# Optimization experiments

Measured on AMD Instinct MI355X. Metric: run time of the kernel, lower is better.

The kernel has to match this reference:

```python
import jax, jax.numpy as jnp
import numpy as np

IN_FEATURES = 1024
N_CLASSES = 50257
CUTOFFS = [2000, 10000]      # head covers [0,2000); clusters [2000,10000), [10000,50257)
DIV_VALUE = 4.0
IGNORE_INDEX = -1
N_ROWS = 4096
HEAD_SIZE = CUTOFFS[0] + len(CUTOFFS)  # 2002 (head classes + one slot per tail cluster)
HSZ = [int(IN_FEATURES // (DIV_VALUE ** (i + 1))) for i in range(len(CUTOFFS))]  # [256, 64]
BOUNDS = CUTOFFS + [N_CLASSES]


def setup_inputs() -> dict:
    key = jax.random.key(0)
    ks = jax.random.split(key, 8)
    x = jax.random.normal(ks[0], (N_ROWS, IN_FEATURES), dtype=jnp.float32)
    target = jax.random.randint(ks[1], (N_ROWS,), 0, N_CLASSES, dtype=jnp.int64)
    drop = jax.random.uniform(ks[2], (N_ROWS,)) < 0.1
    target = jnp.where(drop, IGNORE_INDEX, target)
    s = 1.0 / np.sqrt(IN_FEATURES)
    head_w = jax.random.normal(ks[3], (HEAD_SIZE, IN_FEATURES), dtype=jnp.float32) * s
    proj0 = jax.random.normal(ks[4], (HSZ[0], IN_FEATURES), dtype=jnp.float32) * s
    out0 = jax.random.normal(ks[5], (BOUNDS[1] - BOUNDS[0], HSZ[0]), dtype=jnp.float32) * (1.0 / np.sqrt(HSZ[0]))
    proj1 = jax.random.normal(ks[6], (HSZ[1], IN_FEATURES), dtype=jnp.float32) * s
    out1 = jax.random.normal(ks[7], (BOUNDS[2] - BOUNDS[1], HSZ[1]), dtype=jnp.float32) * (1.0 / np.sqrt(HSZ[1]))
    return {"x": x, "target": target, "head_w": head_w,
            "proj0": proj0, "out0": out0, "proj1": proj1, "out1": out1}


def reference(x, target, head_w, proj0, out0, proj1, out1):
    # head: [N, cutoff0 + n_clusters] logits, shared log-softmax
    head_lp = jax.nn.log_softmax(jnp.einsum('nd,hd->nh', x, head_w), axis=-1)
    rows = jnp.arange(x.shape[0])
    valid = target != IGNORE_INDEX
    t = jnp.where(valid, target, 0)

    # head-band targets: log prob directly from head
    t_head = jnp.clip(t, 0, CUTOFFS[0] - 1)
    logp = head_lp[rows, t_head]

    # tail clusters: head cluster-slot logprob + within-cluster logprob
    tails = [(proj0, out0), (proj1, out1)]
    for i, (proj, out) in enumerate(tails):
        low, high = BOUNDS[i], BOUNDS[i + 1]
        # [N, hsz] @ [hsz, osz] -> [N, osz] cluster logits
        cl_lp = jax.nn.log_softmax(
            jnp.einsum('nh,oh->no', jnp.einsum('nd,hd->nh', x, proj), out), axis=-1)
        rel = jnp.clip(t - low, 0, high - low - 1)
        cand = head_lp[:, CUTOFFS[0] + i] + cl_lp[rows, rel]
        logp = jnp.where((t >= low) & (t < high), cand, logp)

    # ignore-index filter + mean == masked mean over valid rows
    vf = valid.astype(logp.dtype)
    loss = -(logp * vf).sum() / vf.sum()
    return loss
```

## Files before the change

### kernel.cpp

```cpp
#include <hip/hip_runtime.h>
#include <hip/hip_bf16.h>

typedef __attribute__((ext_vector_type(8))) short bf16x8;
typedef __attribute__((ext_vector_type(4))) float f32x4;
typedef unsigned short u16;

constexpr int NR      = 4096;
constexpr int INF     = 1024;
constexpr int HEAD_N  = 2002;
constexpr int HEAD_NP = 2048;
constexpr int C0_LO   = 2000, C0_HI = 10000;
constexpr int C0_N    = 8000;
constexpr int C1_N    = 40257;
constexpr int C1_NP   = 40320;
constexpr int K0      = 256;
constexpr int K1      = 64;
constexpr int PCAT    = 320;
constexpr int PCAT_P  = 384;
constexpr int WCAT_R  = HEAD_NP + PCAT_P;
constexpr int IGNORE  = -1;
constexpr float LOG2E = 1.4426950408889634f;
constexpr float LN2   = 0.6931471805599453f;

constexpr int S0      = 50;
constexpr int TPS0    = 5;
constexpr int S1      = 64;
constexpr int TPS1    = 5;
constexpr int NHP     = 32;
constexpr int HEADB   = 512;
constexpr int C1SLOTS = 768;
constexpr int C0SLOTS = 256;
constexpr int MEGA_GRID = HEADB + C1SLOTS + C0SLOTS;

static __device__ __forceinline__ u16 f32_to_bf16(float f) {
    unsigned int u = __float_as_uint(f);
    return (u16)((u + 0x7FFFu + ((u >> 16) & 1u)) >> 16);
}
static __device__ __forceinline__ float bf2f(u16 v) {
    unsigned int u = ((unsigned int)v) << 16;
    return __uint_as_float(u);
}

static __device__ __forceinline__ float fast_exp2(float x) {
#if __has_builtin(__builtin_amdgcn_exp2f)
    return __builtin_amdgcn_exp2f(x);
#else
    return __expf(x * LN2);
#endif
}

static __device__ __forceinline__ void gload_lds16(const u16* g, u16* l) {
    __builtin_amdgcn_global_load_lds(
        (const __attribute__((address_space(1))) unsigned int*)g,
        (__attribute__((address_space(3))) unsigned int*)l, 16, 0, 0);
}

struct CvtSegs { const float* s[6]; u16* d[6]; int n8[6]; float sc[6]; };

__global__ void cvt_compact(CvtSegs segs, const int* __restrict__ tgt,
                            int* __restrict__ c0list, int* __restrict__ c1list,
                            int* __restrict__ crow, int* __restrict__ cnts) {
    if (blockIdx.x == 0) {
        __shared__ int b0s, b1s;
        const int tid = threadIdx.x;
        const int lane = tid & 63;
        if (tid == 0) { b0s = 0; b1s = 0; }
        __syncthreads();
        for (int it = 0; it < NR / 256; ++it) {
            const int r = it * 256 + tid;
            const int t = tgt[r];
            const bool in0 = (t >= C0_LO) && (t < C0_HI);
            const bool in1 = (t >= C0_HI);
            unsigned long long m0 = __ballot(in0);
            unsigned long long m1 = __ballot(in1);
            int base0 = 0, base1 = 0;
            if (lane == 0) {
                base0 = atomicAdd(&b0s, (int)__popcll(m0));
                base1 = atomicAdd(&b1s, (int)__popcll(m1));
            }
            base0 = __shfl(base0, 0, 64);
            base1 = __shfl(base1, 0, 64);
            const unsigned long long lt = (1ULL << lane) - 1ULL;
            if (in0) { int s = base0 + (int)__popcll(m0 & lt); c0list[s] = r; crow[r] = s; }
            else if (in1) { int s = base1 + (int)__popcll(m1 & lt); c1list[s] = r; crow[r] = s; }
            else crow[r] = 0;
        }
        __syncthreads();
        const int c0 = b0s, c1 = b1s;
        const int p0 = (c0 + 127) & ~127;
        const int p1 = (c1 + 255) & ~255;
        if (threadIdx.x == 0) { cnts[0] = c0; cnts[1] = c1; cnts[2] = p0; cnts[3] = p1; }
        for (int i = c0 + (int)threadIdx.x; i < p0; i += 256) c0list[i] = 0;
        for (int i = c1 + (int)threadIdx.x; i < p1; i += 256) c1list[i] = 0;
    }

    const int stride = gridDim.x * blockDim.x;
    const int gid = blockIdx.x * blockDim.x + threadIdx.x;
#pragma unroll
    for (int seg = 0; seg < 6; ++seg) {
        const float4* sp = (const float4*)segs.s[seg];
        bf16x8* dp = (bf16x8*)segs.d[seg];
        const int n8 = segs.n8[seg];
        const float sc = segs.sc[seg];
        for (int i = gid; i < n8; i += stride) {
            float4 a = sp[2 * i], b = sp[2 * i + 1];
            bf16x8 o;
            o[0] = (short)f32_to_bf16(a.x * sc); o[1] = (short)f32_to_bf16(a.y * sc);
            o[2] = (short)f32_to_bf16(a.z * sc); o[3] = (short)f32_to_bf16(a.w * sc);
            o[4] = (short)f32_to_bf16(b.x * sc); o[5] = (short)f32_to_bf16(b.y * sc);
            o[6] = (short)f32_to_bf16(b.z * sc); o[7] = (short)f32_to_bf16(b.w * sc);
            dp[i] = o;
        }
    }
}

__launch_bounds__(256, 2)
__global__ void proj_tile(const u16* __restrict__ A, const u16* __restrict__ B,
                          u16* __restrict__ HB)
{
    constexpr int K = INF;
    __shared__ u16 ldsA[128 * 64];
    __shared__ u16 ldsB[128 * 64];
    const int tid = threadIdx.x, wid = tid >> 6, lane = tid & 63;
    const int wr = wid >> 1, wc = wid & 1;
    const int row0 = blockIdx.x * 128, col0 = blockIdx.y * 128;

    f32x4 acc[4][4];
#pragma unroll
    for (int m = 0; m < 4; ++m)
#pragma unroll
        for (int n = 0; n < 4; ++n) acc[m][n] = (f32x4){0.f, 0.f, 0.f, 0.f};

    const int srow = lane >> 3;
    const int ssw  = (lane & 7) ^ srow;

    for (int ks = 0; ks < K / 64; ++ks) {
        const int k0 = ks * 64;
#pragma unroll
        for (int q = 0; q < 4; ++q) {
            const int c = q * 4 + wid, row = c * 8 + srow;
            gload_lds16(A + (size_t)(row0 + row) * K + k0 + ssw * 8, ldsA + c * 512);
        }
#pragma unroll
        for (int q = 0; q < 4; ++q) {
            const int c = q * 4 + wid, row = c * 8 + srow;
            gload_lds16(B + (size_t)(col0 + row) * K + k0 + ssw * 8, ldsB + c * 512);
        }
        __syncthreads();
        const bf16x8* A8 = (const bf16x8*)ldsA;
        const bf16x8* B8 = (const bf16x8*)ldsB;
        bf16x8 af[4][2], bfr[4][2];
#pragma unroll
        for (int m = 0; m < 4; ++m) {
            const int ar = wr * 64 + m * 16 + (lane & 15);
#pragma unroll
            for (int ks2 = 0; ks2 < 2; ++ks2)
                af[m][ks2] = A8[ar * 8 + ((ks2 * 4 + (lane >> 4)) ^ (ar & 7))];
        }
#pragma unroll
        for (int n = 0; n < 4; ++n) {
            const int br = wc * 64 + n * 16 + (lane & 15);
#pragma unroll
            for (int ks2 = 0; ks2 < 2; ++ks2)
                bfr[n][ks2] = B8[br * 8 + ((ks2 * 4 + (lane >> 4)) ^ (br & 7))];
        }
#pragma unroll
        for (int ks2 = 0; ks2 < 2; ++ks2)
#pragma unroll
            for (int m = 0; m < 4; ++m)
#pragma unroll
                for (int n = 0; n < 4; ++n)
                    acc[m][n] = __builtin_amdgcn_mfma_f32_16x16x32_bf16(
                        af[m][ks2], bfr[n][ks2], acc[m][n], 0, 0, 0);
        __syncthreads();
    }
#pragma unroll
    for (int m = 0; m < 4; ++m)
#pragma unroll
        for (int n = 0; n < 4; ++n) {
            const int col = col0 + wc * 64 + n * 16 + (lane & 15);
            if (col < PCAT) {
#pragma unroll
                for (int r = 0; r < 4; ++r) {
                    const int row = row0 + wr * 64 + m * 16 + (lane >> 4) * 4 + r;
                    HB[(size_t)row * PCAT + col] = f32_to_bf16(acc[m][n][r]);
                }
            }
        }
}

static __device__ void head_section(int rb, int ct,
                                    const u16* __restrict__ A, const u16* __restrict__ B,
                                    const int* __restrict__ tgt,
                                    float* __restrict__ SEHp, float* __restrict__ TL,
                                    u16* ldsA, u16* ldsB)
{
    constexpr int K = INF;
    const int tid = threadIdx.x, wid = tid >> 6, lane = tid & 63;
    const int wr = wid >> 1, wc = wid & 1;
    const int row0 = rb * 128, col0 = ct * 128;

    f32x4 acc[4][4];
#pragma unroll
    for (int m = 0; m < 4; ++m)
#pragma unroll
        for (int n = 0; n < 4; ++n) acc[m][n] = (f32x4){0.f, 0.f, 0.f, 0.f};

    const int srow = lane >> 3;
    const int ssw  = (lane & 7) ^ srow;

    for (int ks = 0; ks < K / 64; ++ks) {
        const int k0 = ks * 64;
#pragma unroll
        for (int q = 0; q < 4; ++q) {
            const int c = q * 4 + wid, row = c * 8 + srow;
            gload_lds16(A + (size_t)(row0 + row) * K + k0 + ssw * 8, ldsA + c * 512);
        }
#pragma unroll
        for (int q = 0; q < 4; ++q) {
            const int c = q * 4 + wid, row = c * 8 + srow;
            gload_lds16(B + (size_t)(col0 + row) * K + k0 + ssw * 8, ldsB + c * 512);
        }
        __syncthreads();
        const bf16x8* A8 = (const bf16x8*)ldsA;
        const bf16x8* B8 = (const bf16x8*)ldsB;
        bf16x8 af[4][2], bfr[4][2];
#pragma unroll
        for (int m = 0; m < 4; ++m) {
            const int ar = wr * 64 + m * 16 + (lane & 15);
#pragma unroll
            for (int ks2 = 0; ks2 < 2; ++ks2)
                af[m][ks2] = A8[ar * 8 + ((ks2 * 4 + (lane >> 4)) ^ (ar & 7))];
        }
#pragma unroll
        for (int n = 0; n < 4; ++n) {
            const int br = wc * 64 + n * 16 + (lane & 15);
#pragma unroll
            for (int ks2 = 0; ks2 < 2; ++ks2)
                bfr[n][ks2] = B8[br * 8 + ((ks2 * 4 + (lane >> 4)) ^ (br & 7))];
        }
#pragma unroll
        for (int ks2 = 0; ks2 < 2; ++ks2)
#pragma unroll
            for (int m = 0; m < 4; ++m)
#pragma unroll
                for (int n = 0; n < 4; ++n)
                    acc[m][n] = __builtin_amdgcn_mfma_f32_16x16x32_bf16(
                        af[m][ks2], bfr[n][ks2], acc[m][n], 0, 0, 0);
        __syncthreads();
    }

    const int slot = ct * 2 + wc;
#pragma unroll
    for (int m = 0; m < 4; ++m) {
        int th[4];
#pragma unroll
        for (int r = 0; r < 4; ++r) {
            const int t = tgt[row0 + wr * 64 + m * 16 + (lane >> 4) * 4 + r];
            th[r] = (t < 0) ? 0 : (t < C0_LO ? t : (t < C0_HI ? C0_LO : C0_LO + 1));
        }
        f32x4 rs = (f32x4){0.f, 0.f, 0.f, 0.f};
#pragma unroll
        for (int n = 0; n < 4; ++n) {
            const int cls = col0 + wc * 64 + n * 16 + (lane & 15);
            if (cls < HEAD_N) {
#pragma unroll
                for (int r = 0; r < 4; ++r) {
                    rs[r] += fast_exp2(acc[m][n][r]);
                    if (th[r] == cls) {
                        const int lrow = wr * 64 + m * 16 + (lane >> 4) * 4 + r;
                        TL[row0 + lrow] = acc[m][n][r];
                    }
                }
            }
        }
#pragma unroll
        for (int msk = 1; msk < 16; msk <<= 1)
#pragma unroll
            for (int r = 0; r < 4; ++r) rs[r] += __shfl_xor(rs[r], msk, 64);
        if ((lane & 15) == 0) {
            const int rbase = row0 + wr * 64 + m * 16 + (lane >> 4) * 4;
#pragma unroll
            for (int r = 0; r < 4; ++r) SEHp[(size_t)slot * NR + rbase + r] = rs[r];
        }
    }
}

template<int K, int CT, int MSETS>
static __device__ void sumexp_section(const u16* __restrict__ Hbase, int ldh,
                                      const int* __restrict__ list,
                                      const u16* __restrict__ W,
                                      int nreal, int ntiles, int tps,
                                      int rb, int split, float* __restrict__ SEp,
                                      u16* lds)
{
    constexpr int NKF   = K / 32;
    constexpr int SLOTS = K / 8;
    constexpr int CHUNKS = CT * K * 2 / 4096;
    constexpr int RPC   = 256 / SLOTS;
    constexpr int NT    = CT / 16;
    constexpr int BROWS = MSETS * 64;

    const int tid = threadIdx.x, wid = tid >> 6, lane = tid & 63;
    const int row0 = rb * BROWS + wid * (MSETS * 16);

    const int t0 = split * tps;
    const int t1 = min(t0 + tps, ntiles);

    bf16x8 afr[MSETS][NKF];
#pragma unroll
    for (int m = 0; m < MSETS; ++m) {
        const int orow = list[row0 + m * 16 + (lane & 15)];
        const u16* hr = Hbase + (size_t)orow * ldh + (lane >> 4) * 8;
#pragma unroll
        for (int kf = 0; kf < NKF; ++kf)
            afr[m][kf] = *(const bf16x8*)(hr + kf * 32);
    }

    float rs[MSETS][4];
#pragma unroll
    for (int m = 0; m < MSETS; ++m)
#pragma unroll
        for (int r = 0; r < 4; ++r) rs[m][r] = 0.f;

    const int trow  = tid / SLOTS;
    const int swoff = ((tid % SLOTS) ^ (trow & 7)) * 8;

    auto STAGE = [&](int t, int buf) {
        const u16* wb = W + (size_t)t * CT * K + (size_t)trow * K + swoff;
        u16* lb = lds + buf * (CT * K) + wid * 512;
#pragma unroll
        for (int c = 0; c < CHUNKS; ++c)
            gload_lds16(wb + (size_t)c * RPC * K, lb + c * 2048);
    };

    int cur = 0;
    STAGE(t0, 0);
    __syncthreads();

    for (int t = t0; t < t1; ++t) {
        if (t + 1 < t1) STAGE(t + 1, cur ^ 1);
        const bf16x8* B8 = (const bf16x8*)(lds + cur * (CT * K));
        const bool full = (t + 1) * CT <= nreal;
#pragma unroll
        for (int n = 0; n < NT; ++n) {
            const int br = n * 16 + (lane & 15);
            bf16x8 bfr[NKF];
#pragma unroll
            for (int kf = 0; kf < NKF; ++kf)
                bfr[kf] = B8[br * SLOTS + ((kf * 4 + (lane >> 4)) ^ (br & 7))];
            f32x4 acc[MSETS];
#pragma unroll
            for (int m = 0; m < MSETS; ++m) acc[m] = (f32x4){0.f, 0.f, 0.f, 0.f};
#pragma unroll
            for (int m = 0; m < MSETS; ++m)
#pragma unroll
                for (int kf = 0; kf < NKF; ++kf)
                    acc[m] = __builtin_amdgcn_mfma_f32_16x16x32_bf16(
                        afr[m][kf], bfr[kf], acc[m], 0, 0, 0);
            if (full || (t * CT + n * 16 + (lane & 15)) < nreal) {
#pragma unroll
                for (int m = 0; m < MSETS; ++m)
#pragma unroll
                    for (int r = 0; r < 4; ++r) rs[m][r] += fast_exp2(acc[m][r]);
            }
        }
        __syncthreads();
        cur ^= 1;
    }

#pragma unroll
    for (int msk = 1; msk < 16; msk <<= 1)
#pragma unroll
        for (int m = 0; m < MSETS; ++m)
#pragma unroll
            for (int r = 0; r < 4; ++r) rs[m][r] += __shfl_xor(rs[m][r], msk, 64);
    if ((lane & 15) == 0) {
        const int rbase = row0 + (lane >> 4) * 4;
#pragma unroll
        for (int m = 0; m < MSETS; ++m)
#pragma unroll
            for (int r = 0; r < 4; ++r)
                SEp[(size_t)split * NR + rbase + m * 16 + r] = rs[m][r];
    }
}

__launch_bounds__(256, 4)
__global__ void mega_kernel(const u16* __restrict__ xb, const u16* __restrict__ whb,
                            const u16* __restrict__ hcatb,
                            const u16* __restrict__ o0b, const u16* __restrict__ o1b,
                            const int* __restrict__ tgt,
                            const int* __restrict__ c0list, const int* __restrict__ c1list,
                            const int* __restrict__ cnts,
                            float* __restrict__ SEHp, float* __restrict__ TL,
                            float* __restrict__ C0p, float* __restrict__ C1p)
{
    __shared__ u16 smem[2][8192];
    const int bid = blockIdx.x;

    if (bid < HEADB) {
        head_section(bid & 31, bid >> 5, xb, whb, tgt, SEHp, TL,
                     smem[0], smem[1]);
    } else if (bid < HEADB + C1SLOTS) {
        const int c = bid - HEADB;
        const int W1 = (cnts[3] >> 8) * S1;
        for (int w = c; w < W1; w += C1SLOTS)
            sumexp_section<K1, 128, 4>(hcatb + 256, PCAT, c1list, o1b,
                                       C1_N, C1_NP / 128, TPS1, w / S1, w % S1, C1p, smem[0]);
    } else {
        const int c = bid - (HEADB + C1SLOTS);
        const int W0 = (cnts[2] >> 7) * S0;
        for (int w = c; w < W0; w += C0SLOTS)
            sumexp_section<K0, 32, 2>(hcatb, PCAT, c0list, o0b,
                                      C0_N, C0_N / 32, TPS0, w / S0, w % S0, C0p, smem[0]);
    }
}

__global__ void epilogue_kernel(const int* __restrict__ tgt, const float* __restrict__ tl,
                                const float* __restrict__ out0, const float* __restrict__ out1,
                                const u16* __restrict__ hcatb,
                                const float* __restrict__ SEHp, const float* __restrict__ C0p,
                                const float* __restrict__ C1p, const int* __restrict__ crow,
                                float* __restrict__ rowlogp, float* __restrict__ rowvalid) {
    const int wid = threadIdx.x >> 6, lane = threadIdx.x & 63;
    const int r = blockIdx.x * 4 + wid;
    const int t = tgt[r];
    const bool valid = (t != IGNORE);
    const int tc = valid ? t : 0;
    const int band = (tc < C0_LO) ? 0 : (tc < C0_HI) ? 1 : 2;
    const int cr = crow[r];

    float p2 = 0.f;
    if (band == 1) {
        const u16* hr = hcatb + (size_t)r * PCAT;
        const float* crp = out0 + (size_t)(tc - C0_LO) * K0;
        for (int k = lane; k < K0; k += 64) p2 += bf2f(hr[k]) * crp[k];
    } else if (band == 2) {
        p2 = bf2f(hcatb[(size_t)r * PCAT + 256 + lane]) * out1[(size_t)(tc - C0_HI) * K1 + lane];
    }
#pragma unroll
    for (int msk = 32; msk >= 1; msk >>= 1) p2 += __shfl_xor(p2, msk, 64);

    float hp = (lane < NHP) ? SEHp[(size_t)lane * NR + r] : 0.f;
    float cp = 0.f;
    if (band == 1 && lane < S0) cp = C0p[(size_t)lane * NR + cr];
    if (band == 2 && lane < S1) cp = C1p[(size_t)lane * NR + cr];
#pragma unroll
    for (int msk = 1; msk < 64; msk <<= 1) {
        hp += __shfl_xor(hp, msk, 64);
        cp += __shfl_xor(cp, msk, 64);
    }

    if (lane == 0) {
        float logp = LN2 * tl[r] - __logf(hp);
        if (band != 0) logp += p2 - __logf(cp);
        rowlogp[r]  = valid ? logp : 0.f;
        rowvalid[r] = valid ? 1.f : 0.f;
    }
}

__global__ void final_reduce(const float* __restrict__ rowlogp,
                             const float* __restrict__ rowvalid, float* __restrict__ out) {
    __shared__ float sl[256], sv[256];
    const int tid = threadIdx.x;
    float a = 0.f, b = 0.f;
    for (int i = tid; i < NR; i += 256) { a += rowlogp[i]; b += rowvalid[i]; }
    sl[tid] = a; sv[tid] = b;
    __syncthreads();
    for (int s = 128; s > 0; s >>= 1) {
        if (tid < s) { sl[tid] += sl[tid + s]; sv[tid] += sv[tid + s]; }
        __syncthreads();
    }
    if (tid == 0) out[0] = -sl[0] / sv[0];
}

extern "C" void kernel_launch(void* const* d_in, const int* in_sizes, int n_in,
                              void* d_out, int out_size, void* d_ws, size_t ws_size,
                              hipStream_t stream) {
    const float* x      = (const float*)d_in[0];
    const int*   tgt    = (const int*)d_in[1];
    const float* head_w = (const float*)d_in[2];
    const float* proj0  = (const float*)d_in[3];
    const float* out0   = (const float*)d_in[4];
    const float* proj1  = (const float*)d_in[5];
    const float* out1   = (const float*)d_in[6];
    float* loss = (float*)d_out;

    char* base = (char*)d_ws;
    size_t off = 0;
    auto alloc = [&](size_t bytes) { char* p = base + off; off += (bytes + 255) & ~(size_t)255; return p; };

    u16* xb    = (u16*)alloc((size_t)NR * INF * 2);
    u16* wcatb = (u16*)alloc((size_t)WCAT_R * INF * 2);
    u16* o0b   = (u16*)alloc((size_t)C0_N * K0 * 2);
    u16* o1b   = (u16*)alloc((size_t)C1_NP * K1 * 2);
    u16* hcatb = (u16*)alloc((size_t)NR * PCAT * 2);
    float* SEHp = (float*)alloc((size_t)NHP * NR * 4);
    float* C0p  = (float*)alloc((size_t)S0 * NR * 4);
    float* C1p  = (float*)alloc((size_t)S1 * NR * 4);
    float* tl   = (float*)alloc((size_t)NR * 4);
    int* c0list = (int*)alloc((size_t)(NR + 256) * 4);
    int* c1list = (int*)alloc((size_t)(NR + 256) * 4);
    int* crow   = (int*)alloc((size_t)NR * 4);
    int* cnts   = (int*)alloc(4 * 4);
    float* rowlogp  = (float*)alloc((size_t)NR * 4);
    float* rowvalid = (float*)alloc((size_t)NR * 4);

    CvtSegs segs;
    segs.s[0] = x;      segs.d[0] = xb;                              segs.n8[0] = NR * INF / 8;      segs.sc[0] = 1.0f;
    segs.s[1] = head_w; segs.d[1] = wcatb;                           segs.n8[1] = HEAD_N * INF / 8;  segs.sc[1] = LOG2E;
    segs.s[2] = proj0;  segs.d[2] = wcatb + (size_t)HEAD_NP * INF;   segs.n8[2] = 256 * INF / 8;     segs.sc[2] = 1.0f;
    segs.s[3] = proj1;  segs.d[3] = wcatb + (size_t)(HEAD_NP + 256) * INF; segs.n8[3] = 64 * INF / 8; segs.sc[3] = 1.0f;
    segs.s[4] = out0;   segs.d[4] = o0b;                             segs.n8[4] = C0_N * K0 / 8;     segs.sc[4] = LOG2E;
    segs.s[5] = out1;   segs.d[5] = o1b;                             segs.n8[5] = C1_N * K1 / 8;     segs.sc[5] = LOG2E;
    cvt_compact<<<2048, 256, 0, stream>>>(segs, tgt, c0list, c1list, crow, cnts);

    proj_tile<<<dim3(32, PCAT_P / 128), 256, 0, stream>>>(xb, wcatb + (size_t)HEAD_NP * INF, hcatb);

    mega_kernel<<<MEGA_GRID, 256, 0, stream>>>(xb, wcatb, hcatb, o0b, o1b, tgt,
                                               c0list, c1list, cnts, SEHp, tl, C0p, C1p);

    epilogue_kernel<<<NR / 4, 256, 0, stream>>>(tgt, tl, out0, out1, hcatb,
                                                SEHp, C0p, C1p, crow, rowlogp, rowvalid);
    final_reduce<<<1, 256, 0, stream>>>(rowlogp, rowvalid, loss);
    (void)in_sizes; (void)n_in; (void)out_size; (void)ws_size;
}
```

Before: 89.15 us.

## Fuse projection GEMM into conversion kernel reading fp32 inputs directly

The separate proj_tile launch is removed. Its GEMM now runs in the first 96 blocks of the conversion kernel, which load fp32 x and proj weights, convert them to bf16 in registers and write them into LDS, so the projection no longer waits for the bf16 copy of x. This drops one kernel launch and the serial dependency, at the cost of redundant fp32 reads of x (three column tiles) and synchronous loads through registers instead of direct global-to-LDS loads. The remaining blocks handle target compaction and the other conversions with a smaller grid-stride.

```diff
diff --git a/kernel.cpp b/kernel.cpp
--- a/kernel.cpp
+++ b/kernel.cpp
@@ -16,8 +16,6 @@
 constexpr int K0      = 256;
 constexpr int K1      = 64;
 constexpr int PCAT    = 320;
-constexpr int PCAT_P  = 384;
-constexpr int WCAT_R  = HEAD_NP + PCAT_P;
 constexpr int IGNORE  = -1;
 constexpr float LOG2E = 1.4426950408889634f;
 constexpr float LN2   = 0.6931471805599453f;
@@ -31,6 +29,8 @@
 constexpr int C1SLOTS = 768;
 constexpr int C0SLOTS = 256;
 constexpr int MEGA_GRID = HEADB + C1SLOTS + C0SLOTS;
+constexpr int NPROJB  = 96;
+constexpr int CVT_GRID = 2048;
 
 static __device__ __forceinline__ u16 f32_to_bf16(float f) {
     unsigned int u = __float_as_uint(f);
@@ -39,6 +39,14 @@
 static __device__ __forceinline__ float bf2f(u16 v) {
     unsigned int u = ((unsigned int)v) << 16;
     return __uint_as_float(u);
+}
+static __device__ __forceinline__ bf16x8 cvt8(float4 a, float4 b, float sc) {
+    bf16x8 o;
+    o[0] = (short)f32_to_bf16(a.x * sc); o[1] = (short)f32_to_bf16(a.y * sc);
+    o[2] = (short)f32_to_bf16(a.z * sc); o[3] = (short)f32_to_bf16(a.w * sc);
+    o[4] = (short)f32_to_bf16(b.x * sc); o[5] = (short)f32_to_bf16(b.y * sc);
+    o[6] = (short)f32_to_bf16(b.z * sc); o[7] = (short)f32_to_bf16(b.w * sc);
+    return o;
 }
 
 static __device__ __forceinline__ float fast_exp2(float x) {
@@ -55,15 +63,100 @@
         (__attribute__((address_space(3))) unsigned int*)l, 16, 0, 0);
 }
 
-struct CvtSegs { const float* s[6]; u16* d[6]; int n8[6]; float sc[6]; };
-
-__global__ void cvt_compact(CvtSegs segs, const int* __restrict__ tgt,
+struct CvtSegs { const float* s[4]; u16* d[4]; int n8[4]; float sc[4]; };
+
+__launch_bounds__(256, 4)
+__global__ void cvt_compact(CvtSegs segs,
+                            const float* __restrict__ x,
+                            const float* __restrict__ proj0, const float* __restrict__ proj1,
+                            u16* __restrict__ hcatb,
+                            const int* __restrict__ tgt,
                             int* __restrict__ c0list, int* __restrict__ c1list,
                             int* __restrict__ crow, int* __restrict__ cnts) {
-    if (blockIdx.x == 0) {
+    __shared__ u16 plds[2][8192];
+    const int bid = blockIdx.x;
+    const int tid = threadIdx.x;
+    const int wid = tid >> 6, lane = tid & 63;
+
+    if (bid < NPROJB) {
+        const int rb = bid & 31, ct = bid >> 5;
+        const int row0 = rb * 128, col0 = ct * 128;
+        const int wr = wid >> 1, wc = wid & 1;
+
+        f32x4 acc[4][4];
+#pragma unroll
+        for (int m = 0; m < 4; ++m)
+#pragma unroll
+            for (int n = 0; n < 4; ++n) acc[m][n] = (f32x4){0.f, 0.f, 0.f, 0.f};
+
+        for (int ks = 0; ks < INF / 64; ++ks) {
+            const int k0 = ks * 64;
+#pragma unroll
+            for (int j = 0; j < 4; ++j) {
+                const int s = tid + j * 256;
+                const int row = s >> 3, sl = s & 7;
+                {
+                    const float* ap = x + (size_t)(row0 + row) * INF + k0 + sl * 8;
+                    ((bf16x8*)plds[0])[row * 8 + (sl ^ (row & 7))] =
+                        cvt8(*(const float4*)ap, *(const float4*)(ap + 4), 1.0f);
+                }
+                {
+                    const int p = col0 + row;
+                    bf16x8 v = {};
+                    if (p < PCAT) {
+                        const float* bp = (p < 256 ? proj0 + (size_t)p * INF
+                                                   : proj1 + (size_t)(p - 256) * INF) + k0 + sl * 8;
+                        v = cvt8(*(const float4*)bp, *(const float4*)(bp + 4), 1.0f);
+                    }
+                    ((bf16x8*)plds[1])[row * 8 + (sl ^ (row & 7))] = v;
+                }
+            }
+            __syncthreads();
+            const bf16x8* A8 = (const bf16x8*)plds[0];
+            const bf16x8* B8 = (const bf16x8*)plds[1];
+            bf16x8 af[4][2], bfr[4][2];
+#pragma unroll
+            for (int m = 0; m < 4; ++m) {
+                const int ar = wr * 64 + m * 16 + (lane & 15);
+#pragma unroll
+                for (int ks2 = 0; ks2 < 2; ++ks2)
+                    af[m][ks2] = A8[ar * 8 + ((ks2 * 4 + (lane >> 4)) ^ (ar & 7))];
+            }
+#pragma unroll
+            for (int n = 0; n < 4; ++n) {
+                const int br = wc * 64 + n * 16 + (lane & 15);
+#pragma unroll
+                for (int ks2 = 0; ks2 < 2; ++ks2)
+                    bfr[n][ks2] = B8[br * 8 + ((ks2 * 4 + (lane >> 4)) ^ (br & 7))];
+            }
+#pragma unroll
+            for (int ks2 = 0; ks2 < 2; ++ks2)
+#pragma unroll
+                for (int m = 0; m < 4; ++m)
+#pragma unroll
+                    for (int n = 0; n < 4; ++n)
+                        acc[m][n] = __builtin_amdgcn_mfma_f32_16x16x32_bf16(
+                            af[m][ks2], bfr[n][ks2], acc[m][n], 0, 0, 0);
+            __syncthreads();
+        }
+#pragma unroll
+        for (int m = 0; m < 4; ++m)
+#pragma unroll
+            for (int n = 0; n < 4; ++n) {
+                const int col = col0 + wc * 64 + n * 16 + (lane & 15);
+                if (col < PCAT) {
+#pragma unroll
+                    for (int r = 0; r < 4; ++r) {
+                        const int row = row0 + wr * 64 + m * 16 + (lane >> 4) * 4 + r;
+                        hcatb[(size_t)row * PCAT + col] = f32_to_bf16(acc[m][n][r]);
+                    }
+                }
+            }
+        return;
+    }
+
+    if (bid == NPROJB) {
         __shared__ int b0s, b1s;
-        const int tid = threadIdx.x;
-        const int lane = tid & 63;
         if (tid == 0) { b0s = 0; b1s = 0; }
         __syncthreads();
         for (int it = 0; it < NR / 256; ++it) {
@@ -89,104 +182,22 @@
         const int c0 = b0s, c1 = b1s;
         const int p0 = (c0 + 127) & ~127;
         const int p1 = (c1 + 255) & ~255;
-        if (threadIdx.x == 0) { cnts[0] = c0; cnts[1] = c1; cnts[2] = p0; cnts[3] = p1; }
-        for (int i = c0 + (int)threadIdx.x; i < p0; i += 256) c0list[i] = 0;
-        for (int i = c1 + (int)threadIdx.x; i < p1; i += 256) c1list[i] = 0;
-    }
-
-    const int stride = gridDim.x * blockDim.x;
-    const int gid = blockIdx.x * blockDim.x + threadIdx.x;
-#pragma unroll
-    for (int seg = 0; seg < 6; ++seg) {
+        if (tid == 0) { cnts[0] = c0; cnts[1] = c1; cnts[2] = p0; cnts[3] = p1; }
+        for (int i = c0 + tid; i < p0; i += 256) c0list[i] = 0;
+        for (int i = c1 + tid; i < p1; i += 256) c1list[i] = 0;
+    }
+
+    const int stride = (CVT_GRID - NPROJB) * 256;
+    const int gid = (bid - NPROJB) * 256 + tid;
+#pragma unroll
+    for (int seg = 0; seg < 4; ++seg) {
         const float4* sp = (const float4*)segs.s[seg];
         bf16x8* dp = (bf16x8*)segs.d[seg];
         const int n8 = segs.n8[seg];
         const float sc = segs.sc[seg];
-        for (int i = gid; i < n8; i += stride) {
-            float4 a = sp[2 * i], b = sp[2 * i + 1];
-            bf16x8 o;
-            o[0] = (short)f32_to_bf16(a.x * sc); o[1] = (short)f32_to_bf16(a.y * sc);
-            o[2] = (short)f32_to_bf16(a.z * sc); o[3] = (short)f32_to_bf16(a.w * sc);
-            o[4] = (short)f32_to_bf16(b.x * sc); o[5] = (short)f32_to_bf16(b.y * sc);
-            o[6] = (short)f32_to_bf16(b.z * sc); o[7] = (short)f32_to_bf16(b.w * sc);
-            dp[i] = o;
-        }
-    }
-}
-
-__launch_bounds__(256, 2)
-__global__ void proj_tile(const u16* __restrict__ A, const u16* __restrict__ B,
-                          u16* __restrict__ HB)
-{
-    constexpr int K = INF;
-    __shared__ u16 ldsA[128 * 64];
-    __shared__ u16 ldsB[128 * 64];
-    const int tid = threadIdx.x, wid = tid >> 6, lane = tid & 63;
-    const int wr = wid >> 1, wc = wid & 1;
-    const int row0 = blockIdx.x * 128, col0 = blockIdx.y * 128;
-
-    f32x4 acc[4][4];
-#pragma unroll
-    for (int m = 0; m < 4; ++m)
-#pragma unroll
-        for (int n = 0; n < 4; ++n) acc[m][n] = (f32x4){0.f, 0.f, 0.f, 0.f};
-
-    const int srow = lane >> 3;
-    const int ssw  = (lane & 7) ^ srow;
-
-    for (int ks = 0; ks < K / 64; ++ks) {
-        const int k0 = ks * 64;
-#pragma unroll
-        for (int q = 0; q < 4; ++q) {
-            const int c = q * 4 + wid, row = c * 8 + srow;
-            gload_lds16(A + (size_t)(row0 + row) * K + k0 + ssw * 8, ldsA + c * 512);
-        }
-#pragma unroll
-        for (int q = 0; q < 4; ++q) {
-            const int c = q * 4 + wid, row = c * 8 + srow;
-            gload_lds16(B + (size_t)(col0 + row) * K + k0 + ssw * 8, ldsB + c * 512);
-        }
-        __syncthreads();
-        const bf16x8* A8 = (const bf16x8*)ldsA;
-        const bf16x8* B8 = (const bf16x8*)ldsB;
-        bf16x8 af[4][2], bfr[4][2];
-#pragma unroll
-        for (int m = 0; m < 4; ++m) {
-            const int ar = wr * 64 + m * 16 + (lane & 15);
-#pragma unroll
-            for (int ks2 = 0; ks2 < 2; ++ks2)
-                af[m][ks2] = A8[ar * 8 + ((ks2 * 4 + (lane >> 4)) ^ (ar & 7))];
-        }
-#pragma unroll
-        for (int n = 0; n < 4; ++n) {
-            const int br = wc * 64 + n * 16 + (lane & 15);
-#pragma unroll
-            for (int ks2 = 0; ks2 < 2; ++ks2)
-                bfr[n][ks2] = B8[br * 8 + ((ks2 * 4 + (lane >> 4)) ^ (br & 7))];
-        }
-#pragma unroll
-        for (int ks2 = 0; ks2 < 2; ++ks2)
-#pragma unroll
-            for (int m = 0; m < 4; ++m)
-#pragma unroll
-                for (int n = 0; n < 4; ++n)
-                    acc[m][n] = __builtin_amdgcn_mfma_f32_16x16x32_bf16(
-                        af[m][ks2], bfr[n][ks2], acc[m][n], 0, 0, 0);
-        __syncthreads();
-    }
-#pragma unroll
-    for (int m = 0; m < 4; ++m)
-#pragma unroll
-        for (int n = 0; n < 4; ++n) {
-            const int col = col0 + wc * 64 + n * 16 + (lane & 15);
-            if (col < PCAT) {
-#pragma unroll
-                for (int r = 0; r < 4; ++r) {
-                    const int row = row0 + wr * 64 + m * 16 + (lane >> 4) * 4 + r;
-                    HB[(size_t)row * PCAT + col] = f32_to_bf16(acc[m][n][r]);
-                }
-            }
-        }
+        for (int i = gid; i < n8; i += stride)
+            dp[i] = cvt8(sp[2 * i], sp[2 * i + 1], sc);
+    }
 }
 
 static __device__ void head_section(int rb, int ct,
@@ -491,7 +502,7 @@
     auto alloc = [&](size_t bytes) { char* p = base + off; off += (bytes + 255) & ~(size_t)255; return p; };
 
     u16* xb    = (u16*)alloc((size_t)NR * INF * 2);
-    u16* wcatb = (u16*)alloc((size_t)WCAT_R * INF * 2);
+    u16* whb   = (u16*)alloc((size_t)HEAD_NP * INF * 2);
     u16* o0b   = (u16*)alloc((size_t)C0_N * K0 * 2);
     u16* o1b   = (u16*)alloc((size_t)C1_NP * K1 * 2);
     u16* hcatb = (u16*)alloc((size_t)NR * PCAT * 2);
@@ -507,17 +518,14 @@
     float* rowvalid = (float*)alloc((size_t)NR * 4);
 
     CvtSegs segs;
-    segs.s[0] = x;      segs.d[0] = xb;                              segs.n8[0] = NR * INF / 8;      segs.sc[0] = 1.0f;
-    segs.s[1] = head_w; segs.d[1] = wcatb;                           segs.n8[1] = HEAD_N * INF / 8;  segs.sc[1] = LOG2E;
-    segs.s[2] = proj0;  segs.d[2] = wcatb + (size_t)HEAD_NP * INF;   segs.n8[2] = 256 * INF / 8;     segs.sc[2] = 1.0f;
-    segs.s[3] = proj1;  segs.d[3] = wcatb + (size_t)(HEAD_NP + 256) * INF; segs.n8[3] = 64 * INF / 8; segs.sc[3] = 1.0f;
-    segs.s[4] = out0;   segs.d[4] = o0b;                             segs.n8[4] = C0_N * K0 / 8;     segs.sc[4] = LOG2E;
-    segs.s[5] = out1;   segs.d[5] = o1b;                             segs.n8[5] = C1_N * K1 / 8;     segs.sc[5] = LOG2E;
-    cvt_compact<<<2048, 256, 0, stream>>>(segs, tgt, c0list, c1list, crow, cnts);
-
-    proj_tile<<<dim3(32, PCAT_P / 128), 256, 0, stream>>>(xb, wcatb + (size_t)HEAD_NP * INF, hcatb);
-
-    mega_kernel<<<MEGA_GRID, 256, 0, stream>>>(xb, wcatb, hcatb, o0b, o1b, tgt,
+    segs.s[0] = x;      segs.d[0] = xb;   segs.n8[0] = NR * INF / 8;      segs.sc[0] = 1.0f;
+    segs.s[1] = head_w; segs.d[1] = whb;  segs.n8[1] = HEAD_N * INF / 8;  segs.sc[1] = LOG2E;
+    segs.s[2] = out0;   segs.d[2] = o0b;  segs.n8[2] = C0_N * K0 / 8;     segs.sc[2] = LOG2E;
+    segs.s[3] = out1;   segs.d[3] = o1b;  segs.n8[3] = C1_N * K1 / 8;     segs.sc[3] = LOG2E;
+    cvt_compact<<<CVT_GRID, 256, 0, stream>>>(segs, x, proj0, proj1, hcatb,
+                                              tgt, c0list, c1list, crow, cnts);
+
+    mega_kernel<<<MEGA_GRID, 256, 0, stream>>>(xb, whb, hcatb, o0b, o1b, tgt,
                                                c0list, c1list, cnts, SEHp, tl, C0p, C1p);
 
     epilogue_kernel<<<NR / 4, 256, 0, stream>>>(tgt, tl, out0, out1, hcatb,
```

Measured after the change: 104.1 us. 16.7% more time.
